# Optimization experiments

Measured on AMD Instinct MI355X. Metric: run time of the kernel, lower is better.

## Reference

```python
import jax, jax.numpy as jnp
import numpy as np

B, L, H, E = 4, 2048, 16, 64  # batch, seq, heads, head_dim (S=L, D=E)


def setup_inputs() -> dict:
    key = jax.random.key(0)
    kq, kk, kv = jax.random.split(key, 3)
    queries = jax.random.normal(kq, (B, L, H, E), dtype=jnp.float32)
    keys = jax.random.normal(kk, (B, L, H, E), dtype=jnp.float32)
    values = jax.random.normal(kv, (B, L, H, E), dtype=jnp.float32)
    return {"queries": queries, "keys": keys, "values": values}


def reference(queries, keys, values):
    Bq, Lq, Hq, Eq = queries.shape
    scale = 1.0 / float(np.sqrt(Eq))
    # scores: [B, H, L, S]
    scores = jnp.einsum('blhe,bshe->bhls', queries, keys)
    # causal mask: forbid attending to future positions (strict upper triangle)
    causal = jnp.triu(jnp.ones((Lq, Lq), dtype=bool), k=1)
    scores = jnp.where(causal[None, None, :, :], -jnp.inf, scores)
    A = jax.nn.softmax(scale * scores, axis=-1)  # dropout p=0 -> identity
    V = jnp.einsum('bhls,bshd->blhd', A, values)  # [B, L, H, D]
    return V
```

## Files before the change

### kernel.cpp

```cpp
#include <hip/hip_runtime.h>
#include <hip/hip_bf16.h>

typedef short bs8 __attribute__((ext_vector_type(8)));
typedef short bs4 __attribute__((ext_vector_type(4)));
typedef float f32x4 __attribute__((ext_vector_type(4)));

#define B_ 4
#define L_ 2048
#define H_ 16
#define E_ 64
#define QT_ 128
#define KT_ 64
#define KSTR 72
#define PSTR 72
#define NEG_INF (-1e30f)
#define SCALE_LOG2E (0.125f * 1.44269504088896340736f)

__device__ __forceinline__ short bf16of(float x) {
  __hip_bfloat16 h = __float2bfloat16(x);
  return *reinterpret_cast<short*>(&h);
}
__device__ __forceinline__ unsigned pk2(float a, float b) {
  return (unsigned)(unsigned short)bf16of(a) |
         ((unsigned)(unsigned short)bf16of(b) << 16);
}

__global__ __launch_bounds__(256) void prep(const float* __restrict__ K,
                                            const float* __restrict__ V,
                                            short* __restrict__ Kb,
                                            short* __restrict__ Vt) {
  __shared__ unsigned int lt[64 * 35];
  const int tid = threadIdx.x;
  if (blockIdx.x < 2048) {
    size_t base = (size_t)blockIdx.x * 256 + tid;
#pragma unroll
    for (int i = 0; i < 2; ++i) {
      size_t u = base + (size_t)i * 524288;
      int e8 = u & 7;
      int h  = (u >> 3) & 15;
      int s  = (u >> 7) & 2047;
      int b  = (int)(u >> 18);
      float4 f0 = *(const float4*)(K + u * 8);
      float4 f1 = *(const float4*)(K + u * 8 + 4);
      bs8 o;
      o[0] = bf16of(f0.x); o[1] = bf16of(f0.y); o[2] = bf16of(f0.z); o[3] = bf16of(f0.w);
      o[4] = bf16of(f1.x); o[5] = bf16of(f1.y); o[6] = bf16of(f1.z); o[7] = bf16of(f1.w);
      *(bs8*)(Kb + (((size_t)(b * 16 + h) * L_ + s) * E_ + e8 * 8)) = o;
    }
  } else {
    int vb = blockIdx.x - 2048;
    int st = vb & 31, bh = vb >> 5;
    int b = bh >> 4, h = bh & 15;
    int s0 = st * 64;
#pragma unroll
    for (int i = 0; i < 2; ++i) {
      int idx = i * 256 + tid;
      int sp = idx >> 4;
      int e4 = idx & 15;
      const float* p0 = V + (((size_t)b * L_ + s0 + 2 * sp) * H_ + h) * E_ + e4 * 4;
      float4 v0 = *(const float4*)p0;
      float4 v1 = *(const float4*)(p0 + H_ * E_);
      lt[(e4 * 4 + 0) * 35 + sp] = pk2(v0.x, v1.x);
      lt[(e4 * 4 + 1) * 35 + sp] = pk2(v0.y, v1.y);
      lt[(e4 * 4 + 2) * 35 + sp] = pk2(v0.z, v1.z);
      lt[(e4 * 4 + 3) * 35 + sp] = pk2(v0.w, v1.w);
    }
    __syncthreads();
#pragma unroll
    for (int i = 0; i < 2; ++i) {
      int idx = i * 256 + tid;
      int e  = idx >> 3;
      int s8 = idx & 7;
      uint4 o;
      o.x = lt[e * 35 + s8 * 4 + 0];
      o.y = lt[e * 35 + s8 * 4 + 1];
      o.z = lt[e * 35 + s8 * 4 + 2];
      o.w = lt[e * 35 + s8 * 4 + 3];
      *(uint4*)(Vt + ((size_t)bh * E_ + e) * L_ + s0 + 8 * s8) = o;
    }
  }
}

__global__ __launch_bounds__(256, 2) void flash_fwd(const float* __restrict__ Q,
                                                    const short* __restrict__ Kb,
                                                    const short* __restrict__ Vt,
                                                    float* __restrict__ O) {
  const int p  = blockIdx.x;
  const int bh = blockIdx.y;
  const int b = bh >> 4, h = bh & 15;
  const int tid = threadIdx.x;
  const int w = tid >> 6;
  const int lane = tid & 63;
  const int quad = lane >> 4;
  const int l16 = lane & 15;

  __shared__ short ldsK[KT_ * KSTR];
  __shared__ short ldsV[E_ * KSTR];
  __shared__ short ldsP[QT_ * PSTR];

  const short* KbBase = Kb + (size_t)bh * L_ * E_;
  const short* VtBase = Vt + (size_t)bh * E_ * L_;

  const int sr = tid >> 3;
  const int sc = (tid & 7) * 8;

  for (int phase = 0; phase < 2; ++phase) {
    const int qt = phase ? (15 - p) : p;
    const int q0 = qt * QT_;
    const int nkt = 2 * qt + 2;

    bs8 aQ[2][2];
#pragma unroll
    for (int st = 0; st < 2; ++st) {
      const int q = q0 + w * 32 + st * 16 + l16;
      const float* qp = Q + (((size_t)b * L_ + q) * H_ + h) * E_ + quad * 8;
#pragma unroll
      for (int c = 0; c < 2; ++c) {
        float4 f0 = *(const float4*)(qp + c * 32);
        float4 f1 = *(const float4*)(qp + c * 32 + 4);
        bs8 a;
        a[0] = bf16of(f0.x * SCALE_LOG2E); a[1] = bf16of(f0.y * SCALE_LOG2E);
        a[2] = bf16of(f0.z * SCALE_LOG2E); a[3] = bf16of(f0.w * SCALE_LOG2E);
        a[4] = bf16of(f1.x * SCALE_LOG2E); a[5] = bf16of(f1.y * SCALE_LOG2E);
        a[6] = bf16of(f1.z * SCALE_LOG2E); a[7] = bf16of(f1.w * SCALE_LOG2E);
        aQ[st][c] = a;
      }
    }

    f32x4 accO[2][4];
    float accLp[2];
#pragma unroll
    for (int st = 0; st < 2; ++st) {
      accLp[st] = 0.f;
#pragma unroll
      for (int nt = 0; nt < 4; ++nt) accO[st][nt] = (f32x4){0.f, 0.f, 0.f, 0.f};
    }

    bs8 pfK[2], pfV[2];
#pragma unroll
    for (int i = 0; i < 2; ++i) {
      pfK[i] = *(const bs8*)(KbBase + (size_t)(sr + 32 * i) * E_ + sc);
      pfV[i] = *(const bs8*)(VtBase + (size_t)(sr + 32 * i) * L_ + sc);
    }

    for (int kt = 0; kt < nkt; ++kt) {
      const int k0 = kt * KT_;
      __syncthreads();

#pragma unroll
      for (int i = 0; i < 2; ++i) {
        *(bs8*)&ldsK[(sr + 32 * i) * KSTR + sc] = pfK[i];
        *(bs8*)&ldsV[(sr + 32 * i) * KSTR + sc] = pfV[i];
      }
      if (kt + 1 < nkt) {
        const int kn = k0 + KT_;
#pragma unroll
        for (int i = 0; i < 2; ++i) {
          pfK[i] = *(const bs8*)(KbBase + (size_t)(kn + sr + 32 * i) * E_ + sc);
          pfV[i] = *(const bs8*)(VtBase + (size_t)(sr + 32 * i) * L_ + kn + sc);
        }
      }
      __syncthreads();

      bool act0 = (k0 <= q0 + w * 32 + 15);
      bool act1 = (k0 <= q0 + w * 32 + 31);

      if (act1) {
        bs8 aK0[4], aK1[4];
#pragma unroll
        for (int mt = 0; mt < 4; ++mt) {
          aK0[mt] = *(const bs8*)&ldsK[(mt * 16 + l16) * KSTR + quad * 8];
          aK1[mt] = *(const bs8*)&ldsK[(mt * 16 + l16) * KSTR + 32 + quad * 8];
        }

#pragma unroll
        for (int st = 0; st < 2; ++st) {
          bool act = st ? act1 : act0;
          if (act) {
            const int qg = q0 + w * 32 + st * 16 + l16;
            const bool diag = (k0 + KT_ - 1 > q0 + w * 32 + st * 16);
            float rs = 0.f;
#pragma unroll
            for (int mt = 0; mt < 4; ++mt) {
              f32x4 acc = (f32x4){0.f, 0.f, 0.f, 0.f};
              acc = __builtin_amdgcn_mfma_f32_16x16x32_bf16(aK0[mt], aQ[st][0], acc, 0, 0, 0);
              acc = __builtin_amdgcn_mfma_f32_16x16x32_bf16(aK1[mt], aQ[st][1], acc, 0, 0, 0);
              if (diag) {
                const int kb = k0 + mt * 16 + quad * 4;
#pragma unroll
                for (int r = 0; r < 4; ++r)
                  if (kb + r > qg) acc[r] = NEG_INF;
              }
              float p0 = exp2f(acc[0]), p1 = exp2f(acc[1]);
              float p2 = exp2f(acc[2]), p3 = exp2f(acc[3]);
              rs += (p0 + p1) + (p2 + p3);
              uint2 pw;
              pw.x = pk2(p0, p1);
              pw.y = pk2(p2, p3);
              *(uint2*)&ldsP[(w * 32 + st * 16 + l16) * PSTR + mt * 16 + quad * 4] = pw;
            }
            accLp[st] += rs;
          }
        }

        __threadfence_block();

        bs8 aP[2][2];
#pragma unroll
        for (int st = 0; st < 2; ++st) {
          if (st ? act1 : act0) {
            const int rowa = w * 32 + st * 16 + l16;
#pragma unroll
            for (int c = 0; c < 2; ++c)
              aP[st][c] = *(const bs8*)&ldsP[rowa * PSTR + c * 32 + quad * 8];
          }
        }
#pragma unroll
        for (int nt = 0; nt < 4; ++nt) {
          bs8 bV0 = *(const bs8*)&ldsV[(nt * 16 + l16) * KSTR + quad * 8];
          bs8 bV1 = *(const bs8*)&ldsV[(nt * 16 + l16) * KSTR + 32 + quad * 8];
#pragma unroll
          for (int st = 0; st < 2; ++st) {
            if (st ? act1 : act0) {
              accO[st][nt] = __builtin_amdgcn_mfma_f32_16x16x32_bf16(aP[st][0], bV0, accO[st][nt], 0, 0, 0);
              accO[st][nt] = __builtin_amdgcn_mfma_f32_16x16x32_bf16(aP[st][1], bV1, accO[st][nt], 0, 0, 0);
            }
          }
        }
      }
    }

#pragma unroll
    for (int st = 0; st < 2; ++st) {
      float lf = accLp[st];
      lf += __shfl_xor(lf, 16, 64);
      lf += __shfl_xor(lf, 32, 64);
      float inv[4];
#pragma unroll
      for (int r = 0; r < 4; ++r)
        inv[r] = 1.f / __shfl(lf, quad * 4 + r, 64);
#pragma unroll
      for (int nt = 0; nt < 4; ++nt) {
        const int q = q0 + w * 32 + st * 16 + quad * 4;
        const int d = nt * 16 + l16;
        float* op = O + (((size_t)b * L_ + q) * H_ + h) * E_ + d;
#pragma unroll
        for (int r = 0; r < 4; ++r)
          op[(size_t)r * H_ * E_] = accO[st][nt][r] * inv[r];
      }
    }
  }
}

extern "C" void kernel_launch(void* const* d_in, const int* in_sizes, int n_in,
                              void* d_out, int out_size, void* d_ws, size_t ws_size,
                              hipStream_t stream) {
  (void)in_sizes; (void)n_in; (void)out_size; (void)ws_size;
  const float* Q = (const float*)d_in[0];
  const float* K = (const float*)d_in[1];
  const float* V = (const float*)d_in[2];
  float* Out = (float*)d_out;
  short* Kb = (short*)d_ws;
  short* Vt = Kb + (size_t)B_ * H_ * L_ * E_;

  prep<<<4096, 256, 0, stream>>>(K, V, Kb, Vt);
  flash_fwd<<<dim3(8, 64), 256, 0, stream>>>(Q, Kb, Vt, Out);
}
```

Before: 200.8 us.

## Keep softmax probabilities in registers and launch one query tile per block

Drops the LDS round trip for the P matrix. The probabilities produced by the QK^T MFMA are fed directly as A operands into 16x16x16 bf16 MFMAs, and V is stored to LDS in a permuted column layout so its operand matches that register layout. It also replaces the paired-phase block (tile p plus tile 15-p) with one query tile per block over a 16x64 grid, heaviest tiles first, and raises the launch-bounds occupancy hint to 3. The trade-off is the smaller MFMA shape, doubling the PV instruction count, plus reliance on the hardware scheduler rather than pairing to balance causal work.

```diff
diff --git a/kernel.cpp b/kernel.cpp
--- a/kernel.cpp
+++ b/kernel.cpp
@@ -12,7 +12,6 @@
 #define QT_ 128
 #define KT_ 64
 #define KSTR 72
-#define PSTR 72
 #define NEG_INF (-1e30f)
 #define SCALE_LOG2E (0.125f * 1.44269504088896340736f)
 
@@ -81,11 +80,11 @@
   }
 }
 
-__global__ __launch_bounds__(256, 2) void flash_fwd(const float* __restrict__ Q,
+__global__ __launch_bounds__(256, 3) void flash_fwd(const float* __restrict__ Q,
                                                     const short* __restrict__ Kb,
                                                     const short* __restrict__ Vt,
                                                     float* __restrict__ O) {
-  const int p  = blockIdx.x;
+  const int qt = 15 - blockIdx.x;
   const int bh = blockIdx.y;
   const int b = bh >> 4, h = bh & 15;
   const int tid = threadIdx.x;
@@ -96,158 +95,156 @@
 
   __shared__ short ldsK[KT_ * KSTR];
   __shared__ short ldsV[E_ * KSTR];
-  __shared__ short ldsP[QT_ * PSTR];
 
   const short* KbBase = Kb + (size_t)bh * L_ * E_;
   const short* VtBase = Vt + (size_t)bh * E_ * L_;
 
   const int sr = tid >> 3;
   const int sc = (tid & 7) * 8;
-
-  for (int phase = 0; phase < 2; ++phase) {
-    const int qt = phase ? (15 - p) : p;
-    const int q0 = qt * QT_;
-    const int nkt = 2 * qt + 2;
-
-    bs8 aQ[2][2];
-#pragma unroll
-    for (int st = 0; st < 2; ++st) {
-      const int q = q0 + w * 32 + st * 16 + l16;
-      const float* qp = Q + (((size_t)b * L_ + q) * H_ + h) * E_ + quad * 8;
-#pragma unroll
-      for (int c = 0; c < 2; ++c) {
-        float4 f0 = *(const float4*)(qp + c * 32);
-        float4 f1 = *(const float4*)(qp + c * 32 + 4);
-        bs8 a;
-        a[0] = bf16of(f0.x * SCALE_LOG2E); a[1] = bf16of(f0.y * SCALE_LOG2E);
-        a[2] = bf16of(f0.z * SCALE_LOG2E); a[3] = bf16of(f0.w * SCALE_LOG2E);
-        a[4] = bf16of(f1.x * SCALE_LOG2E); a[5] = bf16of(f1.y * SCALE_LOG2E);
-        a[6] = bf16of(f1.z * SCALE_LOG2E); a[7] = bf16of(f1.w * SCALE_LOG2E);
-        aQ[st][c] = a;
-      }
-    }
-
-    f32x4 accO[2][4];
-    float accLp[2];
-#pragma unroll
-    for (int st = 0; st < 2; ++st) {
-      accLp[st] = 0.f;
-#pragma unroll
-      for (int nt = 0; nt < 4; ++nt) accO[st][nt] = (f32x4){0.f, 0.f, 0.f, 0.f};
-    }
-
-    bs8 pfK[2], pfV[2];
-#pragma unroll
-    for (int i = 0; i < 2; ++i) {
-      pfK[i] = *(const bs8*)(KbBase + (size_t)(sr + 32 * i) * E_ + sc);
-      pfV[i] = *(const bs8*)(VtBase + (size_t)(sr + 32 * i) * L_ + sc);
-    }
-
-    for (int kt = 0; kt < nkt; ++kt) {
-      const int k0 = kt * KT_;
-      __syncthreads();
-
+  const int kc = tid & 7;
+  const int vc0 = 32 * (kc & 1) + 4 * (kc >> 1);
+
+  const int q0 = qt * QT_;
+  const int nkt = 2 * qt + 2;
+
+  bs8 aQ[2][2];
+#pragma unroll
+  for (int st = 0; st < 2; ++st) {
+    const int q = q0 + w * 32 + st * 16 + l16;
+    const float* qp = Q + (((size_t)b * L_ + q) * H_ + h) * E_ + quad * 8;
+#pragma unroll
+    for (int c = 0; c < 2; ++c) {
+      float4 f0 = *(const float4*)(qp + c * 32);
+      float4 f1 = *(const float4*)(qp + c * 32 + 4);
+      bs8 a;
+      a[0] = bf16of(f0.x * SCALE_LOG2E); a[1] = bf16of(f0.y * SCALE_LOG2E);
+      a[2] = bf16of(f0.z * SCALE_LOG2E); a[3] = bf16of(f0.w * SCALE_LOG2E);
+      a[4] = bf16of(f1.x * SCALE_LOG2E); a[5] = bf16of(f1.y * SCALE_LOG2E);
+      a[6] = bf16of(f1.z * SCALE_LOG2E); a[7] = bf16of(f1.w * SCALE_LOG2E);
+      aQ[st][c] = a;
+    }
+  }
+
+  f32x4 accO[2][4];
+  float accLp[2];
+#pragma unroll
+  for (int st = 0; st < 2; ++st) {
+    accLp[st] = 0.f;
+#pragma unroll
+    for (int nt = 0; nt < 4; ++nt) accO[st][nt] = (f32x4){0.f, 0.f, 0.f, 0.f};
+  }
+
+  bs8 pfK[2], pfV[2];
+#pragma unroll
+  for (int i = 0; i < 2; ++i) {
+    pfK[i] = *(const bs8*)(KbBase + (size_t)(sr + 32 * i) * E_ + sc);
+    pfV[i] = *(const bs8*)(VtBase + (size_t)(sr + 32 * i) * L_ + sc);
+  }
+
+  for (int kt = 0; kt < nkt; ++kt) {
+    const int k0 = kt * KT_;
+    __syncthreads();
+
+#pragma unroll
+    for (int i = 0; i < 2; ++i) {
+      *(bs8*)&ldsK[(sr + 32 * i) * KSTR + sc] = pfK[i];
+      bs4 lo = __builtin_shufflevector(pfV[i], pfV[i], 0, 1, 2, 3);
+      bs4 hi = __builtin_shufflevector(pfV[i], pfV[i], 4, 5, 6, 7);
+      *(bs4*)&ldsV[(sr + 32 * i) * KSTR + vc0] = lo;
+      *(bs4*)&ldsV[(sr + 32 * i) * KSTR + vc0 + 16] = hi;
+    }
+    if (kt + 1 < nkt) {
+      const int kn = k0 + KT_;
 #pragma unroll
       for (int i = 0; i < 2; ++i) {
-        *(bs8*)&ldsK[(sr + 32 * i) * KSTR + sc] = pfK[i];
-        *(bs8*)&ldsV[(sr + 32 * i) * KSTR + sc] = pfV[i];
-      }
-      if (kt + 1 < nkt) {
-        const int kn = k0 + KT_;
-#pragma unroll
-        for (int i = 0; i < 2; ++i) {
-          pfK[i] = *(const bs8*)(KbBase + (size_t)(kn + sr + 32 * i) * E_ + sc);
-          pfV[i] = *(const bs8*)(VtBase + (size_t)(sr + 32 * i) * L_ + kn + sc);
+        pfK[i] = *(const bs8*)(KbBase + (size_t)(kn + sr + 32 * i) * E_ + sc);
+        pfV[i] = *(const bs8*)(VtBase + (size_t)(sr + 32 * i) * L_ + kn + sc);
+      }
+    }
+    __syncthreads();
+
+    bool act0 = (k0 <= q0 + w * 32 + 15);
+    bool act1 = (k0 <= q0 + w * 32 + 31);
+
+    if (act1) {
+      bs8 aK0[4], aK1[4];
+#pragma unroll
+      for (int mt = 0; mt < 4; ++mt) {
+        aK0[mt] = *(const bs8*)&ldsK[(mt * 16 + l16) * KSTR + quad * 8];
+        aK1[mt] = *(const bs8*)&ldsK[(mt * 16 + l16) * KSTR + 32 + quad * 8];
+      }
+
+      bs4 aPf[2][4];
+#pragma unroll
+      for (int st = 0; st < 2; ++st) {
+        bool act = st ? act1 : act0;
+        if (act) {
+          const int qg = q0 + w * 32 + st * 16 + l16;
+          const bool diag = (k0 + KT_ - 1 > q0 + w * 32 + st * 16);
+          float rs = 0.f;
+#pragma unroll
+          for (int mt = 0; mt < 4; ++mt) {
+            f32x4 acc = (f32x4){0.f, 0.f, 0.f, 0.f};
+            acc = __builtin_amdgcn_mfma_f32_16x16x32_bf16(aK0[mt], aQ[st][0], acc, 0, 0, 0);
+            acc = __builtin_amdgcn_mfma_f32_16x16x32_bf16(aK1[mt], aQ[st][1], acc, 0, 0, 0);
+            if (diag) {
+              const int kb = k0 + mt * 16 + quad * 4;
+#pragma unroll
+              for (int r = 0; r < 4; ++r)
+                if (kb + r > qg) acc[r] = NEG_INF;
+            }
+            float p0 = __builtin_amdgcn_exp2f(acc[0]);
+            float p1 = __builtin_amdgcn_exp2f(acc[1]);
+            float p2 = __builtin_amdgcn_exp2f(acc[2]);
+            float p3 = __builtin_amdgcn_exp2f(acc[3]);
+            rs += (p0 + p1) + (p2 + p3);
+            union { unsigned u[2]; bs4 v; } cv;
+            cv.u[0] = pk2(p0, p1);
+            cv.u[1] = pk2(p2, p3);
+            aPf[st][mt] = cv.v;
+          }
+          accLp[st] += rs;
         }
       }
-      __syncthreads();
-
-      bool act0 = (k0 <= q0 + w * 32 + 15);
-      bool act1 = (k0 <= q0 + w * 32 + 31);
-
-      if (act1) {
-        bs8 aK0[4], aK1[4];
-#pragma unroll
-        for (int mt = 0; mt < 4; ++mt) {
-          aK0[mt] = *(const bs8*)&ldsK[(mt * 16 + l16) * KSTR + quad * 8];
-          aK1[mt] = *(const bs8*)&ldsK[(mt * 16 + l16) * KSTR + 32 + quad * 8];
-        }
-
-#pragma unroll
-        for (int st = 0; st < 2; ++st) {
-          bool act = st ? act1 : act0;
-          if (act) {
-            const int qg = q0 + w * 32 + st * 16 + l16;
-            const bool diag = (k0 + KT_ - 1 > q0 + w * 32 + st * 16);
-            float rs = 0.f;
-#pragma unroll
-            for (int mt = 0; mt < 4; ++mt) {
-              f32x4 acc = (f32x4){0.f, 0.f, 0.f, 0.f};
-              acc = __builtin_amdgcn_mfma_f32_16x16x32_bf16(aK0[mt], aQ[st][0], acc, 0, 0, 0);
-              acc = __builtin_amdgcn_mfma_f32_16x16x32_bf16(aK1[mt], aQ[st][1], acc, 0, 0, 0);
-              if (diag) {
-                const int kb = k0 + mt * 16 + quad * 4;
-#pragma unroll
-                for (int r = 0; r < 4; ++r)
-                  if (kb + r > qg) acc[r] = NEG_INF;
-              }
-              float p0 = exp2f(acc[0]), p1 = exp2f(acc[1]);
-              float p2 = exp2f(acc[2]), p3 = exp2f(acc[3]);
-              rs += (p0 + p1) + (p2 + p3);
-              uint2 pw;
-              pw.x = pk2(p0, p1);
-              pw.y = pk2(p2, p3);
-              *(uint2*)&ldsP[(w * 32 + st * 16 + l16) * PSTR + mt * 16 + quad * 4] = pw;
-            }
-            accLp[st] += rs;
-          }
-        }
-
-        __threadfence_block();
-
-        bs8 aP[2][2];
-#pragma unroll
-        for (int st = 0; st < 2; ++st) {
-          if (st ? act1 : act0) {
-            const int rowa = w * 32 + st * 16 + l16;
-#pragma unroll
-            for (int c = 0; c < 2; ++c)
-              aP[st][c] = *(const bs8*)&ldsP[rowa * PSTR + c * 32 + quad * 8];
-          }
-        }
-#pragma unroll
-        for (int nt = 0; nt < 4; ++nt) {
-          bs8 bV0 = *(const bs8*)&ldsV[(nt * 16 + l16) * KSTR + quad * 8];
-          bs8 bV1 = *(const bs8*)&ldsV[(nt * 16 + l16) * KSTR + 32 + quad * 8];
+
+#pragma unroll
+      for (int nt = 0; nt < 4; ++nt) {
+#pragma unroll
+        for (int hf = 0; hf < 2; ++hf) {
+          bs8 bV = *(const bs8*)&ldsV[(nt * 16 + l16) * KSTR + quad * 16 + hf * 8];
+          bs4 blo = __builtin_shufflevector(bV, bV, 0, 1, 2, 3);
+          bs4 bhi = __builtin_shufflevector(bV, bV, 4, 5, 6, 7);
 #pragma unroll
           for (int st = 0; st < 2; ++st) {
             if (st ? act1 : act0) {
-              accO[st][nt] = __builtin_amdgcn_mfma_f32_16x16x32_bf16(aP[st][0], bV0, accO[st][nt], 0, 0, 0);
-              accO[st][nt] = __builtin_amdgcn_mfma_f32_16x16x32_bf16(aP[st][1], bV1, accO[st][nt], 0, 0, 0);
+              accO[st][nt] = __builtin_amdgcn_mfma_f32_16x16x16bf16_1k(
+                  aPf[st][2 * hf], blo, accO[st][nt], 0, 0, 0);
+              accO[st][nt] = __builtin_amdgcn_mfma_f32_16x16x16bf16_1k(
+                  aPf[st][2 * hf + 1], bhi, accO[st][nt], 0, 0, 0);
             }
           }
         }
       }
     }
-
-#pragma unroll
-    for (int st = 0; st < 2; ++st) {
-      float lf = accLp[st];
-      lf += __shfl_xor(lf, 16, 64);
-      lf += __shfl_xor(lf, 32, 64);
-      float inv[4];
+  }
+
+#pragma unroll
+  for (int st = 0; st < 2; ++st) {
+    float lf = accLp[st];
+    lf += __shfl_xor(lf, 16, 64);
+    lf += __shfl_xor(lf, 32, 64);
+    float inv[4];
+#pragma unroll
+    for (int r = 0; r < 4; ++r)
+      inv[r] = 1.f / __shfl(lf, quad * 4 + r, 64);
+#pragma unroll
+    for (int nt = 0; nt < 4; ++nt) {
+      const int q = q0 + w * 32 + st * 16 + quad * 4;
+      const int d = nt * 16 + l16;
+      float* op = O + (((size_t)b * L_ + q) * H_ + h) * E_ + d;
 #pragma unroll
       for (int r = 0; r < 4; ++r)
-        inv[r] = 1.f / __shfl(lf, quad * 4 + r, 64);
-#pragma unroll
-      for (int nt = 0; nt < 4; ++nt) {
-        const int q = q0 + w * 32 + st * 16 + quad * 4;
-        const int d = nt * 16 + l16;
-        float* op = O + (((size_t)b * L_ + q) * H_ + h) * E_ + d;
-#pragma unroll
-        for (int r = 0; r < 4; ++r)
-          op[(size_t)r * H_ * E_] = accO[st][nt][r] * inv[r];
-      }
+        op[(size_t)r * H_ * E_] = accO[st][nt][r] * inv[r];
     }
   }
 }
@@ -264,5 +261,5 @@
   short* Vt = Kb + (size_t)B_ * H_ * L_ * E_;
 
   prep<<<4096, 256, 0, stream>>>(K, V, Kb, Vt);
-  flash_fwd<<<dim3(8, 64), 256, 0, stream>>>(Q, Kb, Vt, Out);
-}
+  flash_fwd<<<dim3(16, 64), 256, 0, stream>>>(Q, Kb, Vt, Out);
+}
```

Result: slower. 221.4 us (+10.3%).
